# Performance work log

Measured on AMD Instinct MI355X. Metric: run time of the kernel, lower is better.

## Reference

```python
import jax, jax.numpy as jnp
import numpy as np

B, S, D_IN, D_OUT = 4, 2048, 1024, 1024


def setup_inputs() -> dict:
    key = jax.random.key(0)
    kx, kq, kk, kv = jax.random.split(key, 4)
    scale = 1.0 / np.sqrt(D_IN)
    return {
        "x": jax.random.normal(kx, (B, S, D_IN), dtype=jnp.float32),
        "W_q": jax.random.normal(kq, (D_IN, D_OUT), dtype=jnp.float32) * scale,
        "W_k": jax.random.normal(kk, (D_IN, D_OUT), dtype=jnp.float32) * scale,
        "W_v": jax.random.normal(kv, (D_IN, D_OUT), dtype=jnp.float32) * scale,
    }


def reference(x, W_q, W_k, W_v):
    # QKV projections (Linear without bias): [B,S,D_out]
    q = jnp.einsum("bsd,de->bse", x, W_q)
    k = jnp.einsum("bsd,de->bse", x, W_k)
    v = jnp.einsum("bsd,de->bse", x, W_v)

    # Raw scores [B,S,S], causal mask (strict upper triangle -> -inf),
    # then scale by sqrt(d_k) and softmax, matching the torch order of ops.
    scores = jnp.einsum("bqd,bkd->bqk", q, k)
    seq = scores.shape[-1]
    causal = jnp.triu(jnp.ones((seq, seq), dtype=bool), k=1)
    scores = jnp.where(causal[None, :, :], -jnp.inf, scores)
    attn = jax.nn.softmax(scores / jnp.sqrt(jnp.asarray(q.shape[-1], scores.dtype)), axis=-1)
    # dropout p=0.0 -> identity (eval semantics)
    return jnp.einsum("bqk,bkd->bqd", attn, v)
```

## Files before the change

kernel.cpp:

```cpp
#include <hip/hip_runtime.h>

typedef unsigned short u16;
typedef __bf16 bf16x8 __attribute__((ext_vector_type(8)));
typedef float f32x4 __attribute__((ext_vector_type(4)));

__device__ __forceinline__ u16 f2bf(float f) {
    union { float f; unsigned int u; } v; v.f = f;
    unsigned int u = v.u;
    return (u16)((u + 0x7FFFu + ((u >> 16) & 1u)) >> 16);
}

__device__ __forceinline__ void load_lds16(const void* g, void* l) {
    __builtin_amdgcn_global_load_lds(
        (const __attribute__((address_space(1))) unsigned int*)g,
        (__attribute__((address_space(3))) unsigned int*)l,
        16, 0, 0);
}

__global__ void __launch_bounds__(256) prep_kernel(
    const float4* __restrict__ X, u16* __restrict__ xb,
    const float* __restrict__ Wq, const float* __restrict__ Wk,
    const float* __restrict__ Wv,
    u16* __restrict__ Oq, u16* __restrict__ Ok, u16* __restrict__ Ov,
    float* __restrict__ rowsum) {
    __shared__ float tile[32][33];
    const int bid = blockIdx.x, tid = threadIdx.x;
    if (bid < 8192) {
        int idx = bid * 256 + tid;
        float4 v = X[idx];
        ushort4 o;
        o.x = f2bf(v.x); o.y = f2bf(v.y); o.z = f2bf(v.z); o.w = f2bf(v.w);
        *(ushort4*)(xb + (size_t)idx * 4) = o;
    } else if (bid < 11264) {
        int id = bid - 8192;
        int zz = id >> 10;
        const float* W = (zz == 0) ? Wq : (zz == 1) ? Wk : Wv;
        u16* O = (zz == 0) ? Oq : (zz == 1) ? Ok : Ov;
        int n0 = (id & 31) * 32, k0 = ((id >> 5) & 31) * 32;
        int tx = tid & 31, ty = tid >> 5;
        #pragma unroll
        for (int j = 0; j < 32; j += 8)
            tile[ty + j][tx] = W[(size_t)(k0 + ty + j) * 1024 + n0 + tx];
        __syncthreads();
        #pragma unroll
        for (int j = 0; j < 32; j += 8)
            O[(size_t)(n0 + ty + j) * 1024 + k0 + tx] = f2bf(tile[tx][ty + j]);
    } else {
        rowsum[(bid - 11264) * 256 + tid] = 0.f;
    }
}

template <int MODE>
__global__ void __launch_bounds__(512) gemm_nt(
    const u16* __restrict__ xb, const u16* __restrict__ WqT,
    const u16* __restrict__ WkT, const u16* __restrict__ WvT,
    u16* __restrict__ Q, u16* __restrict__ Kb,
    u16* __restrict__ Vt, u16* __restrict__ S,
    float* __restrict__ rowsum, float* __restrict__ out) {

    int mtile, ntile, z;
    const u16 *A, *B;

    if (MODE == 0) {
        int L = blockIdx.x;
        int c = L & 7, t = (L >> 3) & 7, hi = L >> 6;
        int p = hi * 8 + c;
        z = p >> 6; mtile = p & 63; ntile = t;
        A = xb;
        B = (z == 0) ? WqT : (z == 1) ? WkT : WvT;
    } else if (MODE == 1) {
        int id2 = blockIdx.x;
        z = id2 / 192;
        int r = id2 - z * 192;
        int c = r & 7, g = r >> 3;
        if (g <= c)            { mtile = c;     ntile = g; }
        else if (g < 2*c + 10) { mtile = c + 8; ntile = g - (c + 1); }
        else return;
        A = Q  + (size_t)z * (2048 * 1024);
        B = Kb + (size_t)z * (2048 * 1024);
    } else {
        int L = blockIdx.x;
        ntile = L & 7;
        int j = L >> 3;
        z = j & 3; mtile = 15 - (j >> 2);
        A = S  + (size_t)z * (2048 * 2048);
        B = Vt + (size_t)z * (1024 * 2048);
    }

    const int LDA = (MODE == 2) ? 2048 : 1024;
    const int kiters = (MODE == 2) ? (mtile + 1) * 2 : 16;

    __shared__ __align__(16) u16 As[128 * 64];
    __shared__ __align__(16) u16 Bs[128 * 64];

    const int tid = threadIdx.x;
    const int lane = tid & 63;
    const int wave = tid >> 6;
    const int wr = wave >> 2, wc = wave & 3;

    const int r0 = tid >> 2;
    const int kb = (((tid & 3) ^ ((r0 >> 1) & 3))) * 16;

    const char* gA = (const char*)(A + (size_t)(mtile * 128 + r0) * LDA) + kb;
    const char* gB = (const char*)(B + (size_t)(ntile * 128 + r0) * LDA) + kb;

    char* lA = (char*)As + tid * 16;
    char* lB = (char*)Bs + tid * 16;

    f32x4 acc[4][2] = {};

    const int quad = lane >> 4;
    const int l16 = lane & 15;
    const int ch = quad ^ ((l16 >> 1) & 3);
    const int aoff = (wr * 64 + l16) * 32 + ch * 8;
    const int boff = (wc * 32 + l16) * 32 + ch * 8;

    for (int kt = 0; kt < kiters; ++kt) {
        load_lds16(gA,      lA);
        load_lds16(gA + 64, lA + 8192);
        load_lds16(gB,      lB);
        load_lds16(gB + 64, lB + 8192);
        gA += 128; gB += 128;
        __syncthreads();

        #pragma unroll
        for (int h = 0; h < 2; ++h) {
            const u16* ap = As + h * 4096 + aoff;
            const u16* bp = Bs + h * 4096 + boff;
            bf16x8 af[4], bfv[2];
            #pragma unroll
            for (int r = 0; r < 4; ++r) af[r] = *(const bf16x8*)(ap + r * 512);
            #pragma unroll
            for (int c = 0; c < 2; ++c) bfv[c] = *(const bf16x8*)(bp + c * 512);
            #pragma unroll
            for (int r = 0; r < 4; ++r)
                #pragma unroll
                for (int c = 0; c < 2; ++c)
                    acc[r][c] = __builtin_amdgcn_mfma_f32_16x16x32_bf16(
                        af[r], bfv[c], acc[r][c], 0, 0, 0);
        }
        __syncthreads();
    }

    const int grow0 = mtile * 128 + wr * 64 + quad * 4;
    const int gcol0 = ntile * 128 + wc * 32 + l16;

    if (MODE == 0) {
        if (z < 2) {
            u16* C = z ? Kb : Q;
            #pragma unroll
            for (int r = 0; r < 4; ++r)
                #pragma unroll
                for (int c = 0; c < 2; ++c)
                    #pragma unroll
                    for (int i = 0; i < 4; ++i)
                        C[(size_t)(grow0 + r * 16 + i) * 1024 + gcol0 + c * 16] =
                            f2bf(acc[r][c][i]);
        } else {
            #pragma unroll
            for (int r = 0; r < 4; ++r) {
                int m0 = grow0 + r * 16;
                int b = m0 >> 11, s0 = m0 & 2047;
                #pragma unroll
                for (int c = 0; c < 2; ++c) {
                    int d = gcol0 + c * 16;
                    ushort4 o;
                    o.x = f2bf(acc[r][c][0]); o.y = f2bf(acc[r][c][1]);
                    o.z = f2bf(acc[r][c][2]); o.w = f2bf(acc[r][c][3]);
                    *(ushort4*)(Vt + (size_t)b * (1024 * 2048) + (size_t)d * 2048 + s0) = o;
                }
            }
        }
    } else if (MODE == 1) {
        u16* C = S + (size_t)z * (2048 * 2048);
        float* rs = rowsum + z * 2048;
        const bool diag = (ntile == mtile);
        float rsum[4][4];
        #pragma unroll
        for (int r = 0; r < 4; ++r)
            #pragma unroll
            for (int i = 0; i < 4; ++i) rsum[r][i] = 0.f;
        #pragma unroll
        for (int r = 0; r < 4; ++r)
            #pragma unroll
            for (int c = 0; c < 2; ++c)
                #pragma unroll
                for (int i = 0; i < 4; ++i) {
                    int grow = grow0 + r * 16 + i;
                    int gcol = gcol0 + c * 16;
                    float e = 0.f;
                    if (!diag || gcol <= grow)
                        e = __expf(acc[r][c][i] * 0.03125f - 12.0f);
                    C[(size_t)grow * 2048 + gcol] = f2bf(e);
                    rsum[r][i] += e;
                }
        #pragma unroll
        for (int r = 0; r < 4; ++r)
            #pragma unroll
            for (int i = 0; i < 4; ++i) {
                float s = rsum[r][i];
                s += __shfl_xor(s, 1, 64);
                s += __shfl_xor(s, 2, 64);
                s += __shfl_xor(s, 4, 64);
                s += __shfl_xor(s, 8, 64);
                if (l16 == 0)
                    atomicAdd(&rs[grow0 + r * 16 + i], s);
            }
    } else {
        const float* rs = rowsum + z * 2048;
        float* C = out + (size_t)z * (2048 * 1024);
        #pragma unroll
        for (int r = 0; r < 4; ++r)
            #pragma unroll
            for (int i = 0; i < 4; ++i) {
                int grow = grow0 + r * 16 + i;
                float inv = 1.0f / rs[grow];
                #pragma unroll
                for (int c = 0; c < 2; ++c)
                    C[(size_t)grow * 1024 + gcol0 + c * 16] = acc[r][c][i] * inv;
            }
    }
}

extern "C" void kernel_launch(void* const* d_in, const int* in_sizes, int n_in,
                              void* d_out, int out_size, void* d_ws, size_t ws_size,
                              hipStream_t stream) {
    const float* x  = (const float*)d_in[0];
    const float* Wq = (const float*)d_in[1];
    const float* Wk = (const float*)d_in[2];
    const float* Wv = (const float*)d_in[3];
    float* out = (float*)d_out;
    char* ws = (char*)d_ws;
    const size_t Mi = 1u << 20;

    u16* xb  = (u16*)(ws);
    u16* WqT = (u16*)(ws + 16 * Mi);
    u16* WkT = (u16*)(ws + 18 * Mi);
    u16* WvT = (u16*)(ws + 20 * Mi);
    u16* Q   = (u16*)(ws + 22 * Mi);
    u16* Kb  = (u16*)(ws + 38 * Mi);
    u16* Vt  = (u16*)(ws + 54 * Mi);
    u16* S   = (u16*)(ws + 70 * Mi);
    float* rowsum = (float*)(ws + 102 * Mi);

    prep_kernel<<<11296, 256, 0, stream>>>(
        (const float4*)x, xb, Wq, Wk, Wv, WqT, WkT, WvT, rowsum);

    gemm_nt<0><<<1536, 512, 0, stream>>>(xb, WqT, WkT, WvT, Q, Kb, Vt, S, rowsum, out);

    gemm_nt<1><<<768, 512, 0, stream>>>(xb, WqT, WkT, WvT, Q, Kb, Vt, S, rowsum, out);

    gemm_nt<2><<<512, 512, 0, stream>>>(xb, WqT, WkT, WvT, Q, Kb, Vt, S, rowsum, out);
}
```

Baseline: 222.5 us.

## Split attention GEMMs into 64-row tile kernels with finer causal granularity

Separates the QKV projection into its own kernel and moves the QK^T and PV GEMMs into a new 256-thread kernel using 64x128 tiles. The smaller M tile cuts wasted work on the causal triangle, since row blocks now skip more masked columns and PV k-loops scale with 64-row granularity. It also raises block count for better load balance. In exchange, each block reuses less data per load and the causal mask check now runs on every tile.

```diff
diff --git a/kernel.cpp b/kernel.cpp
--- a/kernel.cpp
+++ b/kernel.cpp
@@ -50,48 +50,20 @@
     }
 }
 
-template <int MODE>
-__global__ void __launch_bounds__(512) gemm_nt(
+__global__ void __launch_bounds__(512) gemm_qkv(
     const u16* __restrict__ xb, const u16* __restrict__ WqT,
     const u16* __restrict__ WkT, const u16* __restrict__ WvT,
-    u16* __restrict__ Q, u16* __restrict__ Kb,
-    u16* __restrict__ Vt, u16* __restrict__ S,
-    float* __restrict__ rowsum, float* __restrict__ out) {
-
-    int mtile, ntile, z;
-    const u16 *A, *B;
-
-    if (MODE == 0) {
-        int L = blockIdx.x;
-        int c = L & 7, t = (L >> 3) & 7, hi = L >> 6;
-        int p = hi * 8 + c;
-        z = p >> 6; mtile = p & 63; ntile = t;
-        A = xb;
-        B = (z == 0) ? WqT : (z == 1) ? WkT : WvT;
-    } else if (MODE == 1) {
-        int id2 = blockIdx.x;
-        z = id2 / 192;
-        int r = id2 - z * 192;
-        int c = r & 7, g = r >> 3;
-        if (g <= c)            { mtile = c;     ntile = g; }
-        else if (g < 2*c + 10) { mtile = c + 8; ntile = g - (c + 1); }
-        else return;
-        A = Q  + (size_t)z * (2048 * 1024);
-        B = Kb + (size_t)z * (2048 * 1024);
-    } else {
-        int L = blockIdx.x;
-        ntile = L & 7;
-        int j = L >> 3;
-        z = j & 3; mtile = 15 - (j >> 2);
-        A = S  + (size_t)z * (2048 * 2048);
-        B = Vt + (size_t)z * (1024 * 2048);
-    }
-
-    const int LDA = (MODE == 2) ? 2048 : 1024;
-    const int kiters = (MODE == 2) ? (mtile + 1) * 2 : 16;
-
-    __shared__ __align__(16) u16 As[128 * 64];
-    __shared__ __align__(16) u16 Bs[128 * 64];
+    u16* __restrict__ Q, u16* __restrict__ Kb, u16* __restrict__ Vt) {
+
+    int L = blockIdx.x;
+    int c = L & 7, t = (L >> 3) & 7, hi = L >> 6;
+    int p = hi * 8 + c;
+    const int z = p >> 6, mtile = p & 63, ntile = t;
+    const u16* A = xb;
+    const u16* B = (z == 0) ? WqT : (z == 1) ? WkT : WvT;
+
+    __shared__ __align__(16) u16 As[2 * 128 * 32];
+    __shared__ __align__(16) u16 Bs[2 * 128 * 32];
 
     const int tid = threadIdx.x;
     const int lane = tid & 63;
@@ -101,9 +73,8 @@
     const int r0 = tid >> 2;
     const int kb = (((tid & 3) ^ ((r0 >> 1) & 3))) * 16;
 
-    const char* gA = (const char*)(A + (size_t)(mtile * 128 + r0) * LDA) + kb;
-    const char* gB = (const char*)(B + (size_t)(ntile * 128 + r0) * LDA) + kb;
-
+    const char* gA = (const char*)(A + (size_t)(mtile * 128 + r0) * 1024) + kb;
+    const char* gB = (const char*)(B + (size_t)(ntile * 128 + r0) * 1024) + kb;
     char* lA = (char*)As + tid * 16;
     char* lB = (char*)Bs + tid * 16;
 
@@ -115,14 +86,13 @@
     const int aoff = (wr * 64 + l16) * 32 + ch * 8;
     const int boff = (wc * 32 + l16) * 32 + ch * 8;
 
-    for (int kt = 0; kt < kiters; ++kt) {
+    for (int kt = 0; kt < 16; ++kt) {
         load_lds16(gA,      lA);
         load_lds16(gA + 64, lA + 8192);
         load_lds16(gB,      lB);
         load_lds16(gB + 64, lB + 8192);
         gA += 128; gB += 128;
         __syncthreads();
-
         #pragma unroll
         for (int h = 0; h < 2; ++h) {
             const u16* ap = As + h * 4096 + aoff;
@@ -131,13 +101,13 @@
             #pragma unroll
             for (int r = 0; r < 4; ++r) af[r] = *(const bf16x8*)(ap + r * 512);
             #pragma unroll
-            for (int c = 0; c < 2; ++c) bfv[c] = *(const bf16x8*)(bp + c * 512);
+            for (int cc = 0; cc < 2; ++cc) bfv[cc] = *(const bf16x8*)(bp + cc * 512);
             #pragma unroll
             for (int r = 0; r < 4; ++r)
                 #pragma unroll
-                for (int c = 0; c < 2; ++c)
-                    acc[r][c] = __builtin_amdgcn_mfma_f32_16x16x32_bf16(
-                        af[r], bfv[c], acc[r][c], 0, 0, 0);
+                for (int cc = 0; cc < 2; ++cc)
+                    acc[r][cc] = __builtin_amdgcn_mfma_f32_16x16x32_bf16(
+                        af[r], bfv[cc], acc[r][cc], 0, 0, 0);
         }
         __syncthreads();
     }
@@ -145,36 +115,123 @@
     const int grow0 = mtile * 128 + wr * 64 + quad * 4;
     const int gcol0 = ntile * 128 + wc * 32 + l16;
 
-    if (MODE == 0) {
-        if (z < 2) {
-            u16* C = z ? Kb : Q;
-            #pragma unroll
-            for (int r = 0; r < 4; ++r)
-                #pragma unroll
-                for (int c = 0; c < 2; ++c)
-                    #pragma unroll
-                    for (int i = 0; i < 4; ++i)
-                        C[(size_t)(grow0 + r * 16 + i) * 1024 + gcol0 + c * 16] =
-                            f2bf(acc[r][c][i]);
-        } else {
-            #pragma unroll
-            for (int r = 0; r < 4; ++r) {
-                int m0 = grow0 + r * 16;
-                int b = m0 >> 11, s0 = m0 & 2047;
-                #pragma unroll
-                for (int c = 0; c < 2; ++c) {
-                    int d = gcol0 + c * 16;
-                    ushort4 o;
-                    o.x = f2bf(acc[r][c][0]); o.y = f2bf(acc[r][c][1]);
-                    o.z = f2bf(acc[r][c][2]); o.w = f2bf(acc[r][c][3]);
-                    *(ushort4*)(Vt + (size_t)b * (1024 * 2048) + (size_t)d * 2048 + s0) = o;
-                }
+    if (z < 2) {
+        u16* C = z ? Kb : Q;
+        #pragma unroll
+        for (int r = 0; r < 4; ++r)
+            #pragma unroll
+            for (int cc = 0; cc < 2; ++cc)
+                #pragma unroll
+                for (int i = 0; i < 4; ++i)
+                    C[(size_t)(grow0 + r * 16 + i) * 1024 + gcol0 + cc * 16] =
+                        f2bf(acc[r][cc][i]);
+    } else {
+        #pragma unroll
+        for (int r = 0; r < 4; ++r) {
+            int m0 = grow0 + r * 16;
+            int b = m0 >> 11, s0 = m0 & 2047;
+            #pragma unroll
+            for (int cc = 0; cc < 2; ++cc) {
+                int d = gcol0 + cc * 16;
+                ushort4 o;
+                o.x = f2bf(acc[r][cc][0]); o.y = f2bf(acc[r][cc][1]);
+                o.z = f2bf(acc[r][cc][2]); o.w = f2bf(acc[r][cc][3]);
+                *(ushort4*)(Vt + (size_t)b * (1024 * 2048) + (size_t)d * 2048 + s0) = o;
             }
         }
-    } else if (MODE == 1) {
+    }
+}
+
+template <int MODE>
+__global__ void __launch_bounds__(256) gemm_small(
+    const u16* __restrict__ Q, const u16* __restrict__ Kb,
+    const u16* __restrict__ Vt, u16* __restrict__ S,
+    float* __restrict__ rowsum, float* __restrict__ out) {
+
+    int g, ntile, z, kiters;
+    const u16 *A, *B;
+
+    if (MODE == 1) {
+        int L = blockIdx.x;
+        int p = L & 63;
+        g = L >> 6;
+        z = p >> 4;
+        ntile = p & 15;
+        if (ntile > (g >> 1)) return;
+        kiters = 16;
+        A = Q  + (size_t)z * (2048 * 1024);
+        B = Kb + (size_t)z * (2048 * 1024);
+    } else {
+        int L = blockIdx.x;
+        int p = L & 31;
+        g = 31 - (L >> 5);
+        z = p >> 3;
+        ntile = p & 7;
+        kiters = g + 1;
+        A = S  + (size_t)z * (2048 * 2048);
+        B = Vt + (size_t)z * (1024 * 2048);
+    }
+
+    const int LD = (MODE == 2) ? 2048 : 1024;
+
+    __shared__ __align__(16) u16 As[2 * 64 * 32];
+    __shared__ __align__(16) u16 Bs[2 * 128 * 32];
+
+    const int tid = threadIdx.x;
+    const int lane = tid & 63;
+    const int wc = tid >> 6;
+    const int r0 = tid >> 2;
+    const int kb = (((tid & 3) ^ ((r0 >> 1) & 3))) * 16;
+
+    const char* gA  = (const char*)(A + (size_t)(g * 64 + r0) * LD) + kb;
+    const char* gB0 = (const char*)(B + (size_t)(ntile * 128 + r0) * LD) + kb;
+    const char* gB1 = gB0 + (size_t)64 * LD * 2;
+
+    char* lA = (char*)As + tid * 16;
+    char* lB = (char*)Bs + tid * 16;
+
+    f32x4 acc[4][2] = {};
+
+    const int quad = lane >> 4;
+    const int l16 = lane & 15;
+    const int ch = quad ^ ((l16 >> 1) & 3);
+    const int aoff = l16 * 32 + ch * 8;
+    const int boff = (wc * 32 + l16) * 32 + ch * 8;
+
+    for (int kt = 0; kt < kiters; ++kt) {
+        #pragma unroll
+        for (int h = 0; h < 2; ++h) {
+            load_lds16(gA  + h * 64, lA + h * 4096);
+            load_lds16(gB0 + h * 64, lB + h * 8192);
+            load_lds16(gB1 + h * 64, lB + h * 8192 + 4096);
+        }
+        gA += 128; gB0 += 128; gB1 += 128;
+        __syncthreads();
+        #pragma unroll
+        for (int h = 0; h < 2; ++h) {
+            const u16* ap = As + h * 2048 + aoff;
+            const u16* bp = Bs + h * 4096 + boff;
+            bf16x8 af[4], bfv[2];
+            #pragma unroll
+            for (int r = 0; r < 4; ++r) af[r] = *(const bf16x8*)(ap + r * 512);
+            #pragma unroll
+            for (int cc = 0; cc < 2; ++cc) bfv[cc] = *(const bf16x8*)(bp + cc * 512);
+            #pragma unroll
+            for (int r = 0; r < 4; ++r)
+                #pragma unroll
+                for (int cc = 0; cc < 2; ++cc)
+                    acc[r][cc] = __builtin_amdgcn_mfma_f32_16x16x32_bf16(
+                        af[r], bfv[cc], acc[r][cc], 0, 0, 0);
+        }
+        __syncthreads();
+    }
+
+    const int grow0 = g * 64 + quad * 4;
+    const int gcol0 = ntile * 128 + wc * 32 + l16;
+
+    if (MODE == 1) {
         u16* C = S + (size_t)z * (2048 * 2048);
         float* rs = rowsum + z * 2048;
-        const bool diag = (ntile == mtile);
         float rsum[4][4];
         #pragma unroll
         for (int r = 0; r < 4; ++r)
@@ -183,14 +240,14 @@
         #pragma unroll
         for (int r = 0; r < 4; ++r)
             #pragma unroll
-            for (int c = 0; c < 2; ++c)
+            for (int cc = 0; cc < 2; ++cc)
                 #pragma unroll
                 for (int i = 0; i < 4; ++i) {
                     int grow = grow0 + r * 16 + i;
-                    int gcol = gcol0 + c * 16;
-                    float e = 0.f;
-                    if (!diag || gcol <= grow)
-                        e = __expf(acc[r][c][i] * 0.03125f - 12.0f);
+                    int gcol = gcol0 + cc * 16;
+                    float e = (gcol <= grow)
+                                  ? __expf(acc[r][cc][i] * 0.03125f - 12.0f)
+                                  : 0.f;
                     C[(size_t)grow * 2048 + gcol] = f2bf(e);
                     rsum[r][i] += e;
                 }
@@ -216,8 +273,8 @@
                 int grow = grow0 + r * 16 + i;
                 float inv = 1.0f / rs[grow];
                 #pragma unroll
-                for (int c = 0; c < 2; ++c)
-                    C[(size_t)grow * 1024 + gcol0 + c * 16] = acc[r][c][i] * inv;
+                for (int cc = 0; cc < 2; ++cc)
+                    C[(size_t)grow * 1024 + gcol0 + cc * 16] = acc[r][cc][i] * inv;
             }
     }
 }
@@ -246,9 +303,9 @@
     prep_kernel<<<11296, 256, 0, stream>>>(
         (const float4*)x, xb, Wq, Wk, Wv, WqT, WkT, WvT, rowsum);
 
-    gemm_nt<0><<<1536, 512, 0, stream>>>(xb, WqT, WkT, WvT, Q, Kb, Vt, S, rowsum, out);
-
-    gemm_nt<1><<<768, 512, 0, stream>>>(xb, WqT, WkT, WvT, Q, Kb, Vt, S, rowsum, out);
-
-    gemm_nt<2><<<512, 512, 0, stream>>>(xb, WqT, WkT, WvT, Q, Kb, Vt, S, rowsum, out);
-}
+    gemm_qkv<<<1536, 512, 0, stream>>>(xb, WqT, WkT, WvT, Q, Kb, Vt);
+
+    gemm_small<1><<<2048, 256, 0, stream>>>(Q, Kb, Vt, S, rowsum, out);
+
+    gemm_small<2><<<1024, 256, 0, stream>>>(Q, Kb, Vt, S, rowsum, out);
+}
```

After: 246.5 us. 1.11x slower.
